# Optimization experiments

Measured on AMD Instinct MI355X. Metric: run time of the kernel, lower is better.

Reference implementation:

```python
import jax, jax.numpy as jnp
import numpy as np

B, S, H, NH = 2, 2048, 128, 8  # batch, seq, num_hidden (= per-head dim), num_heads
LN_EPS = 1e-5


def _ln(x, g, b):
    m = jnp.mean(x, axis=-1, keepdims=True)
    v = jnp.var(x, axis=-1, keepdims=True)
    return (x - m) / jnp.sqrt(v + LN_EPS) * g + b


def setup_inputs() -> dict:
    key = jax.random.key(0)
    ks = jax.random.split(key, 18)
    sc = 0.02
    d = {}
    d["x"] = jax.random.normal(ks[0], (B, S, H), jnp.float32)
    # per-head full-dim projections, stacked over heads: [NH, H, H] (in->out layout)
    d["Wq"] = jax.random.normal(ks[1], (NH, H, H), jnp.float32) * sc
    d["bq"] = jax.random.normal(ks[2], (NH, H), jnp.float32) * sc
    d["Wk"] = jax.random.normal(ks[3], (NH, H, H), jnp.float32) * sc
    d["bk"] = jax.random.normal(ks[4], (NH, H), jnp.float32) * sc
    d["Wv"] = jax.random.normal(ks[5], (NH, H, H), jnp.float32) * sc
    d["bv"] = jax.random.normal(ks[6], (NH, H), jnp.float32) * sc
    d["Wo"] = jax.random.normal(ks[7], (NH * H, H), jnp.float32) * sc
    d["bo"] = jax.random.normal(ks[8], (H,), jnp.float32) * sc
    # conv1x1 FFN == pointwise linears: [H, 2H] and [2H, H]
    d["W1"] = jax.random.normal(ks[9], (H, 2 * H), jnp.float32) * sc
    d["b1"] = jax.random.normal(ks[10], (2 * H,), jnp.float32) * sc
    d["W2"] = jax.random.normal(ks[11], (2 * H, H), jnp.float32) * sc
    d["b2"] = jax.random.normal(ks[12], (H,), jnp.float32) * sc
    d["g1"] = jnp.ones((H,), jnp.float32)
    d["beta1"] = jnp.zeros((H,), jnp.float32)
    d["g2"] = jnp.ones((H,), jnp.float32)
    d["beta2"] = jnp.zeros((H,), jnp.float32)
    return d


def reference(x, Wq, bq, Wk, bk, Wv, bv, Wo, bo, W1, b1, W2, b2, g1, beta1, g2, beta2):
    # Multi-head attention: each head uses the FULL embed dim (faithful to source).
    Q = jnp.einsum('bsd,hde->bhse', x, Wq) + bq[None, :, None, :]
    K = jnp.einsum('bsd,hde->bhse', x, Wk) + bk[None, :, None, :]
    V = jnp.einsum('bsd,hde->bhse', x, Wv) + bv[None, :, None, :]
    scores = jnp.einsum('bhse,bhte->bhst', Q, K) / jnp.sqrt(jnp.float32(H))
    A = jax.nn.softmax(scores, axis=-1)          # [B, NH, S, S]
    o = jnp.einsum('bhst,bhte->bhse', A, V)      # [B, NH, S, H]
    o = o.transpose(0, 2, 1, 3).reshape(x.shape[0], x.shape[1], NH * H)  # concat heads
    y = o @ Wo + bo                               # W_O projection
    y = _ln(y, g1, beta1)                         # norm1 (no residual around attn, per source)
    f = jax.nn.relu(jax.nn.relu(y @ W1 + b1) @ W2 + b2)  # conv1x1 -> relu -> conv1x1 -> relu
    y = _ln(y + f, g2, beta2)                     # residual + norm2
    return y
```

## Files before the change

kernel.cpp:

```cpp
#include <hip/hip_runtime.h>
#include <math.h>

#define Bq  2
#define Sq  2048
#define Hq  128
#define NHq 8

typedef __attribute__((ext_vector_type(8))) short bf16x8;
typedef __attribute__((ext_vector_type(4))) float f32x4;
typedef __attribute__((ext_vector_type(16))) float f32x16;
typedef __attribute__((ext_vector_type(4))) unsigned short ushort4_t;
typedef __attribute__((ext_vector_type(4))) unsigned int uint4v;
typedef __attribute__((ext_vector_type(2))) unsigned long long u64x2;
typedef unsigned short ushort_t;
typedef unsigned int uint_t;
typedef unsigned long long u64;

__device__ inline ushort_t f2bf(float f) {
    union { float f; uint_t u; } c; c.f = f;
    uint_t u = c.u + 0x7FFFu + ((c.u >> 16) & 1u);
    return (ushort_t)(u >> 16);
}
__device__ inline float bf2f(ushort_t u) {
    union { uint_t u; float f; } c; c.u = ((uint_t)u) << 16;
    return c.f;
}

__device__ inline uint_t cvtpk_bf16(float lo, float hi) {
    uint_t r;
    asm("v_cvt_pk_bf16_f32 %0, %1, %2" : "=v"(r) : "v"(lo), "v"(hi));
    return r;
}
__device__ inline void pswap32(uint_t &a, uint_t &b) {
    asm("v_permlane32_swap_b32 %0, %1" : "+v"(a), "+v"(b));
}

#define GLOAD16(gsrc, ldst) \
    __builtin_amdgcn_global_load_lds( \
        (const __attribute__((address_space(1))) unsigned int*)(const void*)(gsrc), \
        (__attribute__((address_space(3))) unsigned int*)(ldst), 16, 0, 0)

__global__ __launch_bounds__(256) void tw_kernel(
    const float* __restrict__ Wq, const float* __restrict__ Wk, const float* __restrict__ Wv,
    const float* __restrict__ Wo, const float* __restrict__ W1, const float* __restrict__ W2,
    const float* __restrict__ x,
    ushort_t* __restrict__ Wt_all, ushort_t* __restrict__ Wot,
    ushort_t* __restrict__ W1t, ushort_t* __restrict__ W2t, ushort_t* __restrict__ xb)
{
    const int z = blockIdx.y;
    const int t = threadIdx.x;

    if (z == 27) {
        const int r0 = blockIdx.x << 5;
        #pragma unroll
        for (int i = 0; i < 2; ++i) {
            const int c = t + i * 256;
            const int row = r0 + (c >> 4), j = (c & 15) * 8;
            const float* xp = x + (size_t)row * 128 + j;
            const float4 a = *(const float4*)xp;
            const float4 b = *(const float4*)(xp + 4);
            bf16x8 v;
            v[0]=f2bf(a.x); v[1]=f2bf(a.y); v[2]=f2bf(a.z); v[3]=f2bf(a.w);
            v[4]=f2bf(b.x); v[5]=f2bf(b.y); v[6]=f2bf(b.z); v[7]=f2bf(b.w);
            *(bf16x8*)&xb[(size_t)row * 128 + j] = v;
        }
        return;
    }

    const float* src; ushort_t* dst; int R, C;
    if (z < 24) { const int h = z & 7;
        src = (z < 8 ? Wq : z < 16 ? Wk : Wv) + h * 16384;
        dst = Wt_all + z * 16384; R = 128; C = 128;
    } else if (z == 24) { src = Wo; dst = Wot; R = 1024; C = 128; }
    else if (z == 25)   { src = W1; dst = W1t; R = 128;  C = 256; }
    else                { src = W2; dst = W2t; R = 256;  C = 128; }

    const int tpc = C >> 5;
    if ((int)blockIdx.x >= (R >> 5) * tpc) return;
    const int r0 = (blockIdx.x / tpc) << 5;
    const int c0 = (blockIdx.x % tpc) << 5;

    __shared__ float ls[32][33];
    const int lr = t >> 5, lc = t & 31;
    #pragma unroll
    for (int i = 0; i < 4; ++i)
        ls[lr + i * 8][lc] = src[(size_t)(r0 + lr + i * 8) * C + c0 + lc];
    __syncthreads();
    const int wc = t >> 3, wr0 = (t & 7) << 2;
    ushort4_t o4;
    o4[0] = f2bf(ls[wr0 + 0][wc]); o4[1] = f2bf(ls[wr0 + 1][wc]);
    o4[2] = f2bf(ls[wr0 + 2][wc]); o4[3] = f2bf(ls[wr0 + 3][wc]);
    *(ushort4_t*)&dst[(size_t)(c0 + wc) * R + r0 + wr0] = o4;
}

__global__ __launch_bounds__(256) void qkv_gemm(
    const ushort_t* __restrict__ xb, const ushort_t* __restrict__ Wt_all,
    const float* __restrict__ bq, const float* __restrict__ bk, const float* __restrict__ bv,
    ushort_t* __restrict__ Qb, ushort_t* __restrict__ Kb, ushort_t* __restrict__ Vb)
{
    __shared__ ushort_t As[64 * 128];
    __shared__ ushort_t Bs[128 * 128];
    const int tid = threadIdx.x;
    const int w = tid >> 6, l = tid & 63, lg = l >> 4, ln = l & 15;
    const int m0 = blockIdx.x << 6;
    const int z  = blockIdx.y;

    #pragma unroll
    for (int i = 0; i < 4; ++i) {
        const int seg = w * 4 + i;
        const int row = seg * 4 + (l >> 4);
        const int j = (l & 15) ^ (row & 15);
        GLOAD16(xb + (size_t)(m0 + row) * 128 + j * 8, &As[seg * 512]);
    }
    const ushort_t* Wz = Wt_all + (size_t)z * 16384;
    #pragma unroll
    for (int i = 0; i < 8; ++i) {
        const int seg = w * 8 + i;
        const int row = seg * 4 + (l >> 4);
        const int j = (l & 15) ^ (row & 15);
        GLOAD16(Wz + row * 128 + j * 8, &Bs[seg * 512]);
    }
    __syncthreads();

    bf16x8 af[4];
    #pragma unroll
    for (int kc = 0; kc < 4; ++kc)
        af[kc] = *(const bf16x8*)&As[(w * 16 + ln) * 128 + (((kc * 4 + lg) ^ ln) << 3)];

    f32x4 acc[8];
    #pragma unroll
    for (int nt = 0; nt < 8; ++nt) acc[nt] = (f32x4){0.f,0.f,0.f,0.f};
    #pragma unroll
    for (int nt = 0; nt < 8; ++nt)
        #pragma unroll
        for (int kc = 0; kc < 4; ++kc) {
            const bf16x8 bn = *(const bf16x8*)&Bs[(nt * 16 + ln) * 128 + (((kc * 4 + lg) ^ ln) << 3)];
            acc[nt] = __builtin_amdgcn_mfma_f32_16x16x32_bf16(af[kc], bn, acc[nt], 0, 0, 0);
        }

    const float* bias = (z < 8 ? bq : z < 16 ? bk : bv) + (z & 7) * 128;
    ushort_t* outp = (z < 8 ? Qb : z < 16 ? Kb : Vb);
    const float scale = z < 8 ? 0.08838834764831845f : 1.0f;
    const int h = z & 7;
    #pragma unroll
    for (int nt = 0; nt < 8; ++nt) {
        const float bb = bias[nt * 16 + ln];
        #pragma unroll
        for (int j2 = 0; j2 < 4; ++j2) {
            const int r = m0 + w * 16 + lg * 4 + j2;
            const int b = r >> 11, s = r & 2047;
            outp[((size_t)((b << 3) + h) * 2048 + s) * 128 + nt * 16 + ln] =
                f2bf((acc[nt][j2] + bb) * scale);
        }
    }
}

__global__ __launch_bounds__(256, 2) void attn_kernel(
    const ushort_t* __restrict__ Q, const ushort_t* __restrict__ K,
    const ushort_t* __restrict__ V, ushort_t* __restrict__ Opart,
    float2* __restrict__ ml)
{
    __shared__ ushort_t sh[24576];
    ushort_t* Vt = sh + 16384;

    const int tid = threadIdx.x;
    const int w = tid >> 6, l = tid & 63;
    const int ln5 = l & 31, h5 = l >> 5;

    const int id  = blockIdx.x;
    const int id2 = (id & 7) * 128 + (id >> 3);
    const int s   = id2 >> 8;
    const int bh  = (id2 >> 4) & 15;
    const int q0  = (id2 & 15) << 7;
    const int kv0 = s << 9;

    const size_t base = (size_t)bh * Sq * Hq;
    const ushort_t* Qp = Q + base;
    const ushort_t* Kp = K + base + (size_t)kv0 * Hq;
    const ushort_t* Vp = V + base + (size_t)kv0 * Hq;

    bf16x8 qf[8];
    {
        const ushort_t* qrow = Qp + (size_t)(q0 + w * 32 + ln5) * Hq;
        #pragma unroll
        for (int kc = 0; kc < 8; ++kc)
            qf[kc] = *(const bf16x8*)(qrow + kc * 16 + h5 * 8);
    }

    const int kv2 = (tid & 31) * 2;
    const int d8  = (tid >> 5) * 8;

    f32x16 po[4];
    #pragma unroll
    for (int dt = 0; dt < 4; ++dt)
        #pragma unroll
        for (int r = 0; r < 16; ++r) po[dt][r] = 0.f;
    float m_ = -1e30f, l_ = 0.f;

    #define VT_WRITE(dd, pk) { \
        const int R_ = (dd) >> 1; \
        const int sp_ = (((dd) & 1) << 3) + (kv2 >> 3); \
        *(uint_t*)&Vt[R_ * 128 + ((sp_ ^ (R_ & 15)) << 3) + (kv2 & 7)] = (pk); }

    #pragma unroll
    for (int i = 0; i < 4; ++i) {
        const int seg = w * 4 + i;
        const int row = seg * 4 + (l >> 4);
        const int j = (l & 15) ^ (row & 15);
        GLOAD16(Kp + (size_t)row * Hq + j * 8, &sh[seg * 512]);
    }
    bf16x8 va0 = *(const bf16x8*)(Vp + (size_t)kv2 * Hq + d8);
    bf16x8 va1 = *(const bf16x8*)(Vp + (size_t)(kv2 + 1) * Hq + d8);
    bf16x8 vb0 = *(const bf16x8*)(Vp + (size_t)kv2 * Hq + d8 + 64);
    bf16x8 vb1 = *(const bf16x8*)(Vp + (size_t)(kv2 + 1) * Hq + d8 + 64);
    __syncthreads();
    #pragma unroll
    for (int jj = 0; jj < 8; ++jj) {
        VT_WRITE(d8 + jj,      (uint_t)(ushort_t)va0[jj] | ((uint_t)(ushort_t)va1[jj] << 16));
        VT_WRITE(d8 + 64 + jj, (uint_t)(ushort_t)vb0[jj] | ((uint_t)(ushort_t)vb1[jj] << 16));
    }
    __syncthreads();

    const int NT = 512 / 64;
    for (int t = 0; t < NT; ++t) {
        const int buf = t & 1;
        const ushort_t* Ksb = sh + buf * 8192;

        f32x16 st[2];
        #pragma unroll
        for (int mt = 0; mt < 2; ++mt)
            #pragma unroll
            for (int r = 0; r < 16; ++r) st[mt][r] = 0.f;

        __builtin_amdgcn_s_setprio(1);
        #pragma unroll
        for (int kc = 0; kc < 8; ++kc) {
            #pragma unroll
            for (int mt = 0; mt < 2; ++mt) {
                const int row = mt * 32 + ln5;
                const int slot = (kc * 2 + h5) ^ (row & 15);
                const bf16x8 ka = *(const bf16x8*)&Ksb[row * 128 + (slot << 3)];
                st[mt] = __builtin_amdgcn_mfma_f32_32x32x16_bf16(ka, qf[kc], st[mt], 0, 0, 0);
            }
        }
        __builtin_amdgcn_s_setprio(0);

        if (t + 1 < NT) {
            const int k0n = (t + 1) * 64;
            #pragma unroll
            for (int i = 0; i < 4; ++i) {
                const int seg = w * 4 + i;
                const int row = seg * 4 + (l >> 4);
                const int j = (l & 15) ^ (row & 15);
                GLOAD16(Kp + (size_t)(k0n + row) * Hq + j * 8, &sh[(buf ^ 1) * 8192 + seg * 512]);
            }
            va0 = *(const bf16x8*)(Vp + (size_t)(k0n + kv2) * Hq + d8);
            va1 = *(const bf16x8*)(Vp + (size_t)(k0n + kv2 + 1) * Hq + d8);
            vb0 = *(const bf16x8*)(Vp + (size_t)(k0n + kv2) * Hq + d8 + 64);
            vb1 = *(const bf16x8*)(Vp + (size_t)(k0n + kv2 + 1) * Hq + d8 + 64);
        }

        float mxv[16];
        #pragma unroll
        for (int r = 0; r < 16; ++r) mxv[r] = fmaxf(st[0][r], st[1][r]);
        #pragma unroll
        for (int sd = 8; sd >= 1; sd >>= 1)
            #pragma unroll
            for (int i = 0; i < sd; ++i) mxv[i] = fmaxf(mxv[i], mxv[i + sd]);
        float mx = mxv[0];
        mx = fmaxf(mx, __shfl_xor(mx, 32));

        const bool anyup = __any(mx > m_ + 8.0f);
        float sc = 1.0f;
        if (anyup) {
            const float mn = fmaxf(m_, mx);
            sc = __expf(m_ - mn);
            m_ = mn;
        }

        float pe[32];
        #pragma unroll
        for (int mt = 0; mt < 2; ++mt)
            #pragma unroll
            for (int r = 0; r < 16; ++r)
                pe[mt * 16 + r] = __expf(st[mt][r] - m_);

        float sv[16];
        #pragma unroll
        for (int r = 0; r < 16; ++r) sv[r] = pe[r] + pe[16 + r];
        #pragma unroll
        for (int sd = 8; sd >= 1; sd >>= 1)
            #pragma unroll
            for (int i = 0; i < sd; ++i) sv[i] += sv[i + sd];
        float rs = sv[0];
        rs += __shfl_xor(rs, 32);
        l_ = l_ * sc + rs;

        bf16x8 pb[4];
        #pragma unroll
        for (int ks = 0; ks < 4; ++ks) {
            const int o = (ks >> 1) * 16 + (ks & 1) * 8;
            uint_t wA = cvtpk_bf16(pe[o + 0], pe[o + 1]);
            uint_t wB = cvtpk_bf16(pe[o + 4], pe[o + 5]);
            pswap32(wA, wB);
            uint_t wC = cvtpk_bf16(pe[o + 2], pe[o + 3]);
            uint_t wD = cvtpk_bf16(pe[o + 6], pe[o + 7]);
            pswap32(wC, wD);
            uint4v wv; wv[0] = wA; wv[1] = wC; wv[2] = wB; wv[3] = wD;
            pb[ks] = __builtin_bit_cast(bf16x8, wv);
        }

        if (anyup) {
            #pragma unroll
            for (int dt = 0; dt < 4; ++dt)
                #pragma unroll
                for (int r = 0; r < 16; ++r) po[dt][r] *= sc;
        }

        __builtin_amdgcn_s_setprio(1);
        #pragma unroll
        for (int dt = 0; dt < 4; ++dt) {
            #pragma unroll
            for (int ks = 0; ks < 4; ++ks) {
                const int R_ = dt * 16 + (ln5 >> 1);
                const int sp_ = ((ln5 & 1) << 3) + ks * 2 + h5;
                const bf16x8 va = *(const bf16x8*)&Vt[R_ * 128 + ((sp_ ^ (R_ & 15)) << 3)];
                po[dt] = __builtin_amdgcn_mfma_f32_32x32x16_bf16(va, pb[ks], po[dt], 0, 0, 0);
            }
        }
        __builtin_amdgcn_s_setprio(0);

        __syncthreads();
        if (t + 1 < NT) {
            #pragma unroll
            for (int jj = 0; jj < 8; ++jj) {
                VT_WRITE(d8 + jj,      (uint_t)(ushort_t)va0[jj] | ((uint_t)(ushort_t)va1[jj] << 16));
                VT_WRITE(d8 + 64 + jj, (uint_t)(ushort_t)vb0[jj] | ((uint_t)(ushort_t)vb1[jj] << 16));
            }
        }
        __syncthreads();
    }
    #undef VT_WRITE

    char* wb = (char*)sh + w * 8448;
    #pragma unroll
    for (int dt = 0; dt < 4; ++dt)
        #pragma unroll
        for (int r = 0; r < 16; r += 2) {
            const int d = dt * 32 + (r & 3) + 8 * (r >> 2) + 4 * h5;
            const uint_t pk = cvtpk_bf16(po[dt][r], po[dt][r + 1]);
            *(uint_t*)(wb + ln5 * 264 + d * 2) = pk;
        }
    const int rid0 = (s * 16 + bh) * 2048 + q0 + w * 32;
    #pragma unroll
    for (int rb = 0; rb < 8; ++rb) {
        const int qr = rb * 4 + (l >> 4);
        const char* rp = wb + qr * 264 + (l & 15) * 16;
        u64x2 vv;
        vv[0] = *(const u64*)rp;
        vv[1] = *(const u64*)(rp + 8);
        *(u64x2*)(Opart + (size_t)(rid0 + qr) * 128 + (l & 15) * 8) = vv;
    }
    if (h5 == 0)
        ml[rid0 + ln5] = make_float2(m_, l_);
}

__global__ __launch_bounds__(256) void wo_ln_kernel(
    const ushort_t* __restrict__ Opart, const float2* __restrict__ ml,
    const ushort_t* __restrict__ Wot, const float* __restrict__ bo,
    const float* __restrict__ g1, const float* __restrict__ be1,
    float* __restrict__ y, ushort_t* __restrict__ yb)
{
    __shared__ ushort_t As[32 * 128];
    __shared__ ushort_t Bs[128 * 128];
    __shared__ float ybuf[32 * 132];
    const int tid = threadIdx.x;
    const int w = tid >> 6, l = tid & 63, lg = l >> 4, ln = l & 15;
    const int m0 = blockIdx.x << 5;
    const int rw = (w & 1) * 16;
    const int cw = (w >> 1) * 4;

    f32x4 acc[4];
    #pragma unroll
    for (int nt = 0; nt < 4; ++nt) acc[nt] = (f32x4){0.f,0.f,0.f,0.f};

    for (int ks = 0; ks < 8; ++ks) {
        const int k0 = ks << 7;
        #pragma unroll
        for (int i = 0; i < 2; ++i) {
            const int c = tid + i * 256;
            const int row = c >> 4, j = c & 15;
            const int r = m0 + row, b = r >> 11, q = r & 2047;
            const int prow = ((b << 3) + ks) * 2048 + q;
            const float2 e0 = ml[prow];
            const float2 e1 = ml[32768 + prow];
            const float2 e2 = ml[65536 + prow];
            const float2 e3 = ml[98304 + prow];
            const float M = fmaxf(fmaxf(e0.x, e1.x), fmaxf(e2.x, e3.x));
            const float w0 = __expf(e0.x - M), w1 = __expf(e1.x - M);
            const float w2 = __expf(e2.x - M), w3 = __expf(e3.x - M);
            const float inv = 1.0f / (w0 * e0.y + w1 * e1.y + w2 * e2.y + w3 * e3.y);
            const size_t po_ = (size_t)prow * 128 + j * 8;
            const bf16x8 o0 = *(const bf16x8*)&Opart[po_];
            const bf16x8 o1 = *(const bf16x8*)&Opart[po_ + (size_t)32768 * 128];
            const bf16x8 o2 = *(const bf16x8*)&Opart[po_ + (size_t)65536 * 128];
            const bf16x8 o3 = *(const bf16x8*)&Opart[po_ + (size_t)98304 * 128];
            bf16x8 mv;
            #pragma unroll
            for (int jj = 0; jj < 8; ++jj) {
                const float v = (w0 * bf2f((ushort_t)o0[jj]) + w1 * bf2f((ushort_t)o1[jj]) +
                                 w2 * bf2f((ushort_t)o2[jj]) + w3 * bf2f((ushort_t)o3[jj])) * inv;
                mv[jj] = (short)f2bf(v);
            }
            *(bf16x8*)&As[row * 128 + ((j ^ (row & 15)) << 3)] = mv;
        }
        #pragma unroll
        for (int i = 0; i < 8; ++i) {
            const int seg = w * 8 + i;
            const int row = seg * 4 + (l >> 4);
            const int j = (l & 15) ^ (row & 15);
            GLOAD16(Wot + (size_t)row * 1024 + k0 + j * 8, &Bs[seg * 512]);
        }
        __syncthreads();

        bf16x8 af[4];
        #pragma unroll
        for (int kc = 0; kc < 4; ++kc)
            af[kc] = *(const bf16x8*)&As[(rw + ln) * 128 + (((kc * 4 + lg) ^ ln) << 3)];
        #pragma unroll
        for (int nt = 0; nt < 4; ++nt)
            #pragma unroll
            for (int kc = 0; kc < 4; ++kc) {
                const bf16x8 bn = *(const bf16x8*)&Bs[((cw + nt) * 16 + ln) * 128 + (((kc * 4 + lg) ^ ln) << 3)];
                acc[nt] = __builtin_amdgcn_mfma_f32_16x16x32_bf16(af[kc], bn, acc[nt], 0, 0, 0);
            }
        __syncthreads();
    }

    #pragma unroll
    for (int nt = 0; nt < 4; ++nt) {
        const int col = (cw + nt) * 16 + ln;
        const float bb = bo[col];
        #pragma unroll
        for (int j2 = 0; j2 < 4; ++j2)
            ybuf[(rw + lg * 4 + j2) * 132 + col] = acc[nt][j2] + bb;
    }
    __syncthreads();

    const int row = tid >> 3, sub = tid & 7;
    float vals[16];
    float sm = 0.f, sq = 0.f;
    #pragma unroll
    for (int e = 0; e < 16; ++e) {
        const float v = ybuf[row * 132 + sub * 16 + e];
        vals[e] = v; sm += v; sq += v * v;
    }
    #pragma unroll
    for (int mmk = 1; mmk <= 4; mmk <<= 1) {
        sm += __shfl_xor(sm, mmk);
        sq += __shfl_xor(sq, mmk);
    }
    const float mean = sm * (1.0f / 128.0f);
    const float var  = sq * (1.0f / 128.0f) - mean * mean;
    const float rstd = rsqrtf(var + 1e-5f);
    const int r = m0 + row;
    float* yp = y + (size_t)r * 128 + sub * 16;
    ushort_t* ybp = yb + (size_t)r * 128 + sub * 16;
    #pragma unroll
    for (int e = 0; e < 16; e += 2) {
        const int col = sub * 16 + e;
        const float v0 = (vals[e]   - mean) * rstd * g1[col]   + be1[col];
        const float v1 = (vals[e+1] - mean) * rstd * g1[col+1] + be1[col+1];
        yp[e] = v0; yp[e+1] = v1;
        *(uint_t*)&ybp[e] = (uint_t)f2bf(v0) | ((uint_t)f2bf(v1) << 16);
    }
}

__global__ __launch_bounds__(256) void gemm32_kernel(
    const ushort_t* __restrict__ A, const ushort_t* __restrict__ Bt,
    const float* __restrict__ bias, ushort_t* __restrict__ Cb,
    int N, int K, int KS)
{
    __shared__ ushort_t As[32 * 128];
    __shared__ ushort_t Bs[128 * 128];
    const int tid = threadIdx.x;
    const int w = tid >> 6, l = tid & 63, lg = l >> 4, ln = l & 15;
    const int m0 = blockIdx.x << 5;
    const int n0 = blockIdx.y << 7;
    const int rw = (w & 1) * 16;
    const int cw = (w >> 1) * 4;

    f32x4 acc[4];
    #pragma unroll
    for (int nt = 0; nt < 4; ++nt) acc[nt] = (f32x4){0.f,0.f,0.f,0.f};

    for (int ks = 0; ks < KS; ++ks) {
        const int k0 = ks << 7;
        #pragma unroll
        for (int i = 0; i < 2; ++i) {
            const int seg = w * 2 + i;
            const int row = seg * 4 + (l >> 4);
            const int j = (l & 15) ^ (row & 15);
            GLOAD16(A + (size_t)(m0 + row) * K + k0 + j * 8, &As[seg * 512]);
        }
        #pragma unroll
        for (int i = 0; i < 8; ++i) {
            const int seg = w * 8 + i;
            const int row = seg * 4 + (l >> 4);
            const int j = (l & 15) ^ (row & 15);
            GLOAD16(Bt + (size_t)(n0 + row) * K + k0 + j * 8, &Bs[seg * 512]);
        }
        __syncthreads();

        bf16x8 af[4];
        #pragma unroll
        for (int kc = 0; kc < 4; ++kc)
            af[kc] = *(const bf16x8*)&As[(rw + ln) * 128 + (((kc * 4 + lg) ^ ln) << 3)];
        #pragma unroll
        for (int nt = 0; nt < 4; ++nt)
            #pragma unroll
            for (int kc = 0; kc < 4; ++kc) {
                const bf16x8 bn = *(const bf16x8*)&Bs[((cw + nt) * 16 + ln) * 128 + (((kc * 4 + lg) ^ ln) << 3)];
                acc[nt] = __builtin_amdgcn_mfma_f32_16x16x32_bf16(af[kc], bn, acc[nt], 0, 0, 0);
            }
        __syncthreads();
    }

    #pragma unroll
    for (int nt = 0; nt < 4; ++nt) {
        const int col = n0 + (cw + nt) * 16 + ln;
        const float bb = bias[col];
        #pragma unroll
        for (int j2 = 0; j2 < 4; ++j2) {
            const int r = m0 + rw + lg * 4 + j2;
            Cb[(size_t)r * N + col] = f2bf(fmaxf(acc[nt][j2] + bb, 0.f));
        }
    }
}

__global__ __launch_bounds__(256) void ffn2_ln_kernel(
    const ushort_t* __restrict__ h1, const ushort_t* __restrict__ W2t,
    const float* __restrict__ b2, const float* __restrict__ y,
    const float* __restrict__ g2, const float* __restrict__ be2,
    float* __restrict__ out)
{
    __shared__ ushort_t As[32 * 128];
    __shared__ ushort_t Bs[128 * 128];
    __shared__ float ybuf[32 * 132];
    const int tid = threadIdx.x;
    const int w = tid >> 6, l = tid & 63, lg = l >> 4, ln = l & 15;
    const int m0 = blockIdx.x << 5;
    const int rw = (w & 1) * 16;
    const int cw = (w >> 1) * 4;

    f32x4 acc[4];
    #pragma unroll
    for (int nt = 0; nt < 4; ++nt) acc[nt] = (f32x4){0.f,0.f,0.f,0.f};

    for (int ks = 0; ks < 2; ++ks) {
        const int k0 = ks << 7;
        #pragma unroll
        for (int i = 0; i < 2; ++i) {
            const int seg = w * 2 + i;
            const int row = seg * 4 + (l >> 4);
            const int j = (l & 15) ^ (row & 15);
            GLOAD16(h1 + (size_t)(m0 + row) * 256 + k0 + j * 8, &As[seg * 512]);
        }
        #pragma unroll
        for (int i = 0; i < 8; ++i) {
            const int seg = w * 8 + i;
            const int row = seg * 4 + (l >> 4);
            const int j = (l & 15) ^ (row & 15);
            GLOAD16(W2t + (size_t)row * 256 + k0 + j * 8, &Bs[seg * 512]);
        }
        __syncthreads();

        bf16x8 af[4];
        #pragma unroll
        for (int kc = 0; kc < 4; ++kc)
            af[kc] = *(const bf16x8*)&As[(rw + ln) * 128 + (((kc * 4 + lg) ^ ln) << 3)];
        #pragma unroll
        for (int nt = 0; nt < 4; ++nt)
            #pragma unroll
            for (int kc = 0; kc < 4; ++kc) {
                const bf16x8 bn = *(const bf16x8*)&Bs[((cw + nt) * 16 + ln) * 128 + (((kc * 4 + lg) ^ ln) << 3)];
                acc[nt] = __builtin_amdgcn_mfma_f32_16x16x32_bf16(af[kc], bn, acc[nt], 0, 0, 0);
            }
        __syncthreads();
    }

    #pragma unroll
    for (int nt = 0; nt < 4; ++nt) {
        const int col = (cw + nt) * 16 + ln;
        const float bb = b2[col];
        #pragma unroll
        for (int j2 = 0; j2 < 4; ++j2) {
            const int row = rw + lg * 4 + j2;
            const float f = fmaxf(acc[nt][j2] + bb, 0.f);
            ybuf[row * 132 + col] = f + y[(size_t)(m0 + row) * 128 + col];
        }
    }
    __syncthreads();

    const int row = tid >> 3, sub = tid & 7;
    float vals[16];
    float sm = 0.f, sq = 0.f;
    #pragma unroll
    for (int e = 0; e < 16; ++e) {
        const float v = ybuf[row * 132 + sub * 16 + e];
        vals[e] = v; sm += v; sq += v * v;
    }
    #pragma unroll
    for (int mmk = 1; mmk <= 4; mmk <<= 1) {
        sm += __shfl_xor(sm, mmk);
        sq += __shfl_xor(sq, mmk);
    }
    const float mean = sm * (1.0f / 128.0f);
    const float var  = sq * (1.0f / 128.0f) - mean * mean;
    const float rstd = rsqrtf(var + 1e-5f);
    float* op = out + (size_t)(m0 + row) * 128 + sub * 16;
    #pragma unroll
    for (int e = 0; e < 16; ++e) {
        const int col = sub * 16 + e;
        op[e] = (vals[e] - mean) * rstd * g2[col] + be2[col];
    }
}

extern "C" void kernel_launch(void* const* d_in, const int* in_sizes, int n_in,
                              void* d_out, int out_size, void* d_ws, size_t ws_size,
                              hipStream_t stream)
{
    const float* x   = (const float*)d_in[0];
    const float* Wq  = (const float*)d_in[1];
    const float* bq  = (const float*)d_in[2];
    const float* Wk  = (const float*)d_in[3];
    const float* bk  = (const float*)d_in[4];
    const float* Wv  = (const float*)d_in[5];
    const float* bv  = (const float*)d_in[6];
    const float* Wo  = (const float*)d_in[7];
    const float* bo  = (const float*)d_in[8];
    const float* W1  = (const float*)d_in[9];
    const float* b1  = (const float*)d_in[10];
    const float* W2  = (const float*)d_in[11];
    const float* b2  = (const float*)d_in[12];
    const float* g1  = (const float*)d_in[13];
    const float* be1 = (const float*)d_in[14];
    const float* g2  = (const float*)d_in[15];
    const float* be2 = (const float*)d_in[16];
    (void)in_sizes; (void)n_in; (void)out_size; (void)ws_size;

    ushort_t* Wt_all = (ushort_t*)d_ws;
    ushort_t* Wot   = Wt_all + 393216;
    ushort_t* W1t   = Wot + 131072;
    ushort_t* W2t   = W1t + 32768;
    ushort_t* xb    = W2t + 32768;
    ushort_t* Qb    = xb + 524288;
    ushort_t* Kb    = Qb + 4194304;
    ushort_t* Vb    = Kb + 4194304;
    ushort_t* Opart = Vb + 4194304;
    float2*   ml    = (float2*)(Opart + 16777216);
    float*    y  = (float*)Qb;
    ushort_t* yb = Kb;
    ushort_t* h1 = Opart;

    tw_kernel    <<<dim3(128, 28), 256, 0, stream>>>(Wq, Wk, Wv, Wo, W1, W2, x,
                                                     Wt_all, Wot, W1t, W2t, xb);
    qkv_gemm     <<<dim3(64, 24),  256, 0, stream>>>(xb, Wt_all, bq, bk, bv, Qb, Kb, Vb);
    attn_kernel  <<<dim3(1024),    256, 0, stream>>>(Qb, Kb, Vb, Opart, ml);
    wo_ln_kernel <<<dim3(128),     256, 0, stream>>>(Opart, ml, Wot, bo, g1, be1, y, yb);
    gemm32_kernel<<<dim3(128, 2),  256, 0, stream>>>(yb, W1t, b1, h1, 256, 128, 1);
    ffn2_ln_kernel<<<dim3(128),    256, 0, stream>>>(h1, W2t, b2, y, g2, be2, (float*)d_out);
}
```

Measured before the change: 94.33 us.

## Halve attention KV splits and switch V transpose to row-per-dim layout

Measured after the change: 88.15 us. 6.5% less time.

```diff
diff --git a/kernel.cpp b/kernel.cpp
--- a/kernel.cpp
+++ b/kernel.cpp
@@ -160,7 +160,7 @@
     const ushort_t* __restrict__ V, ushort_t* __restrict__ Opart,
     float2* __restrict__ ml)
 {
-    __shared__ ushort_t sh[24576];
+    __shared__ ushort_t sh[32768];
     ushort_t* Vt = sh + 16384;
 
     const int tid = threadIdx.x;
@@ -168,11 +168,11 @@
     const int ln5 = l & 31, h5 = l >> 5;
 
     const int id  = blockIdx.x;
-    const int id2 = (id & 7) * 128 + (id >> 3);
+    const int id2 = (id & 7) * 64 + (id >> 3);
     const int s   = id2 >> 8;
     const int bh  = (id2 >> 4) & 15;
     const int q0  = (id2 & 15) << 7;
-    const int kv0 = s << 9;
+    const int kv0 = s << 10;
 
     const size_t base = (size_t)bh * Sq * Hq;
     const ushort_t* Qp = Q + base;
@@ -196,11 +196,6 @@
         #pragma unroll
         for (int r = 0; r < 16; ++r) po[dt][r] = 0.f;
     float m_ = -1e30f, l_ = 0.f;
-
-    #define VT_WRITE(dd, pk) { \
-        const int R_ = (dd) >> 1; \
-        const int sp_ = (((dd) & 1) << 3) + (kv2 >> 3); \
-        *(uint_t*)&Vt[R_ * 128 + ((sp_ ^ (R_ & 15)) << 3) + (kv2 & 7)] = (pk); }
 
     #pragma unroll
     for (int i = 0; i < 4; ++i) {
@@ -216,12 +211,15 @@
     __syncthreads();
     #pragma unroll
     for (int jj = 0; jj < 8; ++jj) {
-        VT_WRITE(d8 + jj,      (uint_t)(ushort_t)va0[jj] | ((uint_t)(ushort_t)va1[jj] << 16));
-        VT_WRITE(d8 + 64 + jj, (uint_t)(ushort_t)vb0[jj] | ((uint_t)(ushort_t)vb1[jj] << 16));
+        const int r1 = d8 + jj, r2 = d8 + 64 + jj;
+        *(uint_t*)&Vt[r1 * 128 + ((((kv2 >> 3) ^ (r1 & 15))) << 3) + (kv2 & 7)] =
+            (uint_t)(ushort_t)va0[jj] | ((uint_t)(ushort_t)va1[jj] << 16);
+        *(uint_t*)&Vt[r2 * 128 + ((((kv2 >> 3) ^ (r2 & 15))) << 3) + (kv2 & 7)] =
+            (uint_t)(ushort_t)vb0[jj] | ((uint_t)(ushort_t)vb1[jj] << 16);
     }
     __syncthreads();
 
-    const int NT = 512 / 64;
+    const int NT = 1024 / 64;
     for (int t = 0; t < NT; ++t) {
         const int buf = t & 1;
         const ushort_t* Ksb = sh + buf * 8192;
@@ -322,9 +320,9 @@
         for (int dt = 0; dt < 4; ++dt) {
             #pragma unroll
             for (int ks = 0; ks < 4; ++ks) {
-                const int R_ = dt * 16 + (ln5 >> 1);
-                const int sp_ = ((ln5 & 1) << 3) + ks * 2 + h5;
-                const bf16x8 va = *(const bf16x8*)&Vt[R_ * 128 + ((sp_ ^ (R_ & 15)) << 3)];
+                const int row = dt * 32 + ln5;
+                const int slot = (ks * 2 + h5) ^ (row & 15);
+                const bf16x8 va = *(const bf16x8*)&Vt[row * 128 + (slot << 3)];
                 po[dt] = __builtin_amdgcn_mfma_f32_32x32x16_bf16(va, pb[ks], po[dt], 0, 0, 0);
             }
         }
@@ -334,15 +332,18 @@
         if (t + 1 < NT) {
             #pragma unroll
             for (int jj = 0; jj < 8; ++jj) {
-                VT_WRITE(d8 + jj,      (uint_t)(ushort_t)va0[jj] | ((uint_t)(ushort_t)va1[jj] << 16));
-                VT_WRITE(d8 + 64 + jj, (uint_t)(ushort_t)vb0[jj] | ((uint_t)(ushort_t)vb1[jj] << 16));
-            }
-        }
-        __syncthreads();
-    }
-    #undef VT_WRITE
-
-    char* wb = (char*)sh + w * 8448;
+                const int r1 = d8 + jj, r2 = d8 + 64 + jj;
+                *(uint_t*)&Vt[r1 * 128 + ((((kv2 >> 3) ^ (r1 & 15))) << 3) + (kv2 & 7)] =
+                    (uint_t)(ushort_t)va0[jj] | ((uint_t)(ushort_t)va1[jj] << 16);
+                *(uint_t*)&Vt[r2 * 128 + ((((kv2 >> 3) ^ (r2 & 15))) << 3) + (kv2 & 7)] =
+                    (uint_t)(ushort_t)vb0[jj] | ((uint_t)(ushort_t)vb1[jj] << 16);
+            }
+        }
+        __syncthreads();
+    }
+
+    char* shb = (char*)sh;
+    char* wb = shb + w * 8448;
     #pragma unroll
     for (int dt = 0; dt < 4; ++dt)
         #pragma unroll
@@ -394,22 +395,16 @@
             const int prow = ((b << 3) + ks) * 2048 + q;
             const float2 e0 = ml[prow];
             const float2 e1 = ml[32768 + prow];
-            const float2 e2 = ml[65536 + prow];
-            const float2 e3 = ml[98304 + prow];
-            const float M = fmaxf(fmaxf(e0.x, e1.x), fmaxf(e2.x, e3.x));
+            const float M = fmaxf(e0.x, e1.x);
             const float w0 = __expf(e0.x - M), w1 = __expf(e1.x - M);
-            const float w2 = __expf(e2.x - M), w3 = __expf(e3.x - M);
-            const float inv = 1.0f / (w0 * e0.y + w1 * e1.y + w2 * e2.y + w3 * e3.y);
+            const float inv = 1.0f / (w0 * e0.y + w1 * e1.y);
             const size_t po_ = (size_t)prow * 128 + j * 8;
             const bf16x8 o0 = *(const bf16x8*)&Opart[po_];
             const bf16x8 o1 = *(const bf16x8*)&Opart[po_ + (size_t)32768 * 128];
-            const bf16x8 o2 = *(const bf16x8*)&Opart[po_ + (size_t)65536 * 128];
-            const bf16x8 o3 = *(const bf16x8*)&Opart[po_ + (size_t)98304 * 128];
             bf16x8 mv;
             #pragma unroll
             for (int jj = 0; jj < 8; ++jj) {
-                const float v = (w0 * bf2f((ushort_t)o0[jj]) + w1 * bf2f((ushort_t)o1[jj]) +
-                                 w2 * bf2f((ushort_t)o2[jj]) + w3 * bf2f((ushort_t)o3[jj])) * inv;
+                const float v = (w0 * bf2f((ushort_t)o0[jj]) + w1 * bf2f((ushort_t)o1[jj])) * inv;
                 mv[jj] = (short)f2bf(v);
             }
             *(bf16x8*)&As[row * 128 + ((j ^ (row & 15)) << 3)] = mv;
@@ -658,7 +653,7 @@
     ushort_t* Kb    = Qb + 4194304;
     ushort_t* Vb    = Kb + 4194304;
     ushort_t* Opart = Vb + 4194304;
-    float2*   ml    = (float2*)(Opart + 16777216);
+    float2*   ml    = (float2*)(Opart + 8388608);
     float*    y  = (float*)Qb;
     ushort_t* yb = Kb;
     ushort_t* h1 = Opart;
@@ -666,7 +661,7 @@
     tw_kernel    <<<dim3(128, 28), 256, 0, stream>>>(Wq, Wk, Wv, Wo, W1, W2, x,
                                                      Wt_all, Wot, W1t, W2t, xb);
     qkv_gemm     <<<dim3(64, 24),  256, 0, stream>>>(xb, Wt_all, bq, bk, bv, Qb, Kb, Vb);
-    attn_kernel  <<<dim3(1024),    256, 0, stream>>>(Qb, Kb, Vb, Opart, ml);
+    attn_kernel  <<<dim3(512),     256, 0, stream>>>(Qb, Kb, Vb, Opart, ml);
     wo_ln_kernel <<<dim3(128),     256, 0, stream>>>(Opart, ml, Wot, bo, g1, be1, y, yb);
     gemm32_kernel<<<dim3(128, 2),  256, 0, stream>>>(yb, W1t, b1, h1, 256, 128, 1);
     ffn2_ln_kernel<<<dim3(128),    256, 0, stream>>>(h1, W2t, b2, y, g2, be2, (float*)d_out);
```
